# Performance work log

Measured on AMD Instinct MI355X. Metric: run time of the kernel, lower is better.

Reference implementation:

```python
import jax, jax.numpy as jnp
import numpy as np

B, C, KC, H, W, M = 8, 512, 256, 128, 128, 19


def _cbr(x, Wt, s, b):
    # 1x1 conv (no bias) + folded BatchNorm affine + ReLU.  x: [B,Cin,H,W], Wt: [Cout,Cin]
    y = jnp.einsum('oc,bchw->bohw', Wt, x)
    return jax.nn.relu(y * s[None, :, None, None] + b[None, :, None, None])


def setup_inputs() -> dict:
    key = jax.random.key(0)
    ks = jax.random.split(key, 10)
    inp = {
        'x': jax.random.normal(ks[0], (B, C, H, W), jnp.float32),
        'proxy': jax.random.normal(ks[1], (B, C, M, 1), jnp.float32),
    }
    # fan-in scaled weights so activations stay O(1)
    inp['W_p1'] = jax.random.normal(ks[2], (KC, C), jnp.float32) * (C ** -0.5)
    inp['W_p2'] = jax.random.normal(ks[3], (KC, KC), jnp.float32) * (KC ** -0.5)
    inp['W_o1'] = jax.random.normal(ks[4], (KC, C), jnp.float32) * (C ** -0.5)
    inp['W_o2'] = jax.random.normal(ks[5], (KC, KC), jnp.float32) * (KC ** -0.5)
    inp['W_d1'] = jax.random.normal(ks[6], (KC, C), jnp.float32) * (C ** -0.5)
    inp['W_d2'] = jax.random.normal(ks[7], (KC, KC), jnp.float32) * (KC ** -0.5)
    inp['W_u'] = jax.random.normal(ks[8], (C, KC), jnp.float32) * (KC ** -0.5)
    for name, dim in [('p1', KC), ('p2', KC), ('o1', KC), ('o2', KC), ('d1', KC), ('d2', KC), ('u', C)]:
        inp['s_' + name] = jnp.ones((dim,), jnp.float32)
        inp['b_' + name] = jnp.zeros((dim,), jnp.float32)
    return inp


def reference(x, proxy, W_p1, s_p1, b_p1, W_p2, s_p2, b_p2,
              W_o1, s_o1, b_o1, W_o2, s_o2, b_o2,
              W_d1, s_d1, b_d1, W_d2, s_d2, b_d2,
              W_u, s_u, b_u):
    b, _, h, w = x.shape
    kc = W_p1.shape[0]
    # pixel query / object key / object value projections (two ConvBnRelu each)
    q = _cbr(_cbr(x, W_p1, s_p1, b_p1), W_p2, s_p2, b_p2)          # [B,KC,H,W]
    k = _cbr(_cbr(proxy, W_o1, s_o1, b_o1), W_o2, s_o2, b_o2)      # [B,KC,M,1]
    v = _cbr(_cbr(proxy, W_d1, s_d1, b_d1), W_d2, s_d2, b_d2)      # [B,KC,M,1]
    q = q.reshape(b, kc, h * w)                                    # [B,KC,P]
    k = k.reshape(b, kc, -1)                                       # [B,KC,M]
    v = v.reshape(b, kc, -1)                                       # [B,KC,M]
    sim = jnp.einsum('bkp,bkm->bpm', q, k) * (kc ** -0.5)          # [B,P,M]
    sim = jax.nn.softmax(sim, axis=-1)
    ctx = jnp.einsum('bpm,bkm->bkp', sim, v).reshape(b, kc, h, w)  # [B,KC,H,W]
    return _cbr(ctx, W_u, s_u, b_u)                                # [B,C,H,W]
```

## Files before the change

### kernel.cpp

```cpp
#include <hip/hip_runtime.h>
#include <hip/hip_bf16.h>
#include <cstddef>
#include <cstdint>

constexpr int B_  = 8;
constexpr int C_  = 512;
constexpr int KC_ = 256;
constexpr int M_  = 19;
constexpr int P_  = 128 * 128;

typedef short frag8 __attribute__((ext_vector_type(8)));
typedef float f32x4 __attribute__((ext_vector_type(4)));
typedef unsigned short u16x8 __attribute__((ext_vector_type(8)));

__device__ __forceinline__ unsigned pk_bf16(float a, float b) {
    union { __hip_bfloat162 h; unsigned u; } cv;
    cv.h = __float22bfloat162_rn(make_float2(a, b));
    return cv.u;
}
__device__ __forceinline__ ushort bf16_1(float a) {
    union { __hip_bfloat16 h; ushort u; } cv;
    cv.h = __float2bfloat16(a);
    return cv.u;
}
__device__ __forceinline__ float bf16_f(ushort u) {
    return __uint_as_float(((unsigned)u) << 16);
}

__device__ __forceinline__ void gll16(const ushort* g, ushort* l) {
    __builtin_amdgcn_global_load_lds(
        (__attribute__((address_space(1))) void*)(ushort*)g,
        (__attribute__((address_space(3))) void*)l, 16, 0, 0);
}

__device__ __forceinline__ void two_stage_proj(
    const float* __restrict__ pS, float* __restrict__ t1,
    const float* __restrict__ W1, const float* __restrict__ s1, const float* __restrict__ b1,
    const float* __restrict__ W2, const float* __restrict__ s2, const float* __restrict__ b2,
    float* __restrict__ outg, int b, int tid)
{
    float acc[M_];
#pragma unroll
    for (int m = 0; m < M_; ++m) acc[m] = 0.f;
    const float4* wrow = reinterpret_cast<const float4*>(W1 + (size_t)tid * C_);
    for (int c4 = 0; c4 < C_ / 4; ++c4) {
        float4 w = wrow[c4];
        const float* pr = pS + c4 * 4 * M_;
#pragma unroll
        for (int m = 0; m < M_; ++m) acc[m] = fmaf(w.x, pr[m], acc[m]);
#pragma unroll
        for (int m = 0; m < M_; ++m) acc[m] = fmaf(w.y, pr[M_ + m], acc[m]);
#pragma unroll
        for (int m = 0; m < M_; ++m) acc[m] = fmaf(w.z, pr[2 * M_ + m], acc[m]);
#pragma unroll
        for (int m = 0; m < M_; ++m) acc[m] = fmaf(w.w, pr[3 * M_ + m], acc[m]);
    }
    float s = s1[tid], bb = b1[tid];
    __syncthreads();
#pragma unroll
    for (int m = 0; m < M_; ++m) t1[tid * M_ + m] = fmaxf(fmaf(acc[m], s, bb), 0.f);
    __syncthreads();
#pragma unroll
    for (int m = 0; m < M_; ++m) acc[m] = 0.f;
    const float4* wrow2 = reinterpret_cast<const float4*>(W2 + (size_t)tid * KC_);
    for (int c4 = 0; c4 < KC_ / 4; ++c4) {
        float4 w = wrow2[c4];
        const float* tr = t1 + c4 * 4 * M_;
#pragma unroll
        for (int m = 0; m < M_; ++m) acc[m] = fmaf(w.x, tr[m], acc[m]);
#pragma unroll
        for (int m = 0; m < M_; ++m) acc[m] = fmaf(w.y, tr[M_ + m], acc[m]);
#pragma unroll
        for (int m = 0; m < M_; ++m) acc[m] = fmaf(w.z, tr[2 * M_ + m], acc[m]);
#pragma unroll
        for (int m = 0; m < M_; ++m) acc[m] = fmaf(w.w, tr[3 * M_ + m], acc[m]);
    }
    s = s2[tid]; bb = b2[tid];
#pragma unroll
    for (int m = 0; m < M_; ++m)
        outg[((size_t)b * KC_ + tid) * M_ + m] = fmaxf(fmaf(acc[m], s, bb), 0.f);
}

__device__ __forceinline__ void cvt_w(const float* __restrict__ s, ushort* __restrict__ d,
                                      int n4, int cid, int nb) {
    for (int i = cid * 256 + (int)threadIdx.x; i < n4; i += nb * 256) {
        float4 f = ((const float4*)s)[i];
        ushort4 h;
        h.x = bf16_1(f.x); h.y = bf16_1(f.y); h.z = bf16_1(f.z); h.w = bf16_1(f.w);
        ((ushort4*)d)[i] = h;
    }
}

__global__ __launch_bounds__(256) void front_kernel(
    const float* __restrict__ proxy,
    const float* __restrict__ Wo1, const float* __restrict__ so1, const float* __restrict__ bo1,
    const float* __restrict__ Wo2, const float* __restrict__ so2, const float* __restrict__ bo2,
    const float* __restrict__ Wd1, const float* __restrict__ sd1, const float* __restrict__ bd1,
    const float* __restrict__ Wd2, const float* __restrict__ sd2, const float* __restrict__ bd2,
    float* __restrict__ Kg, float* __restrict__ Vg,
    const float* __restrict__ Wp1f, const float* __restrict__ Wp2f, const float* __restrict__ Wuf,
    ushort* __restrict__ Wp1b, ushort* __restrict__ Wp2b, ushort* __restrict__ Wub)
{
    __shared__ float pS[C_ * M_];
    __shared__ float t1[KC_ * M_];
    const int bx = blockIdx.x, tid = threadIdx.x;
    if (bx < 16) {
        const int b = bx >> 1;
        for (int i = tid; i < C_ * M_; i += 256) pS[i] = proxy[(size_t)b * C_ * M_ + i];
        __syncthreads();
        if (bx & 1)
            two_stage_proj(pS, t1, Wd1, sd1, bd1, Wd2, sd2, bd2, Vg, b, tid);
        else
            two_stage_proj(pS, t1, Wo1, so1, bo1, Wo2, so2, bo2, Kg, b, tid);
    } else {
        const int cid = bx - 16, nb = (int)gridDim.x - 16;
        cvt_w(Wp1f, Wp1b, KC_ * C_ / 4, cid, nb);
        cvt_w(Wp2f, Wp2b, KC_ * KC_ / 4, cid, nb);
        cvt_w(Wuf,  Wub,  C_ * KC_ / 4, cid, nb);
    }
}

__global__ __launch_bounds__(256) void cbr_f32in(
    const ushort* __restrict__ Wb, const float* __restrict__ X,
    const float* __restrict__ sc, const float* __restrict__ bi,
    ushort* __restrict__ Y)
{
    constexpr int K = C_;
    constexpr int O = KC_;
    __shared__ __align__(16) ushort As[128][40];
    __shared__ __align__(16) ushort Bs[128][40];

    const int tid = threadIdx.x;
    const unsigned bid = blockIdx.x;
    const unsigned swz = (bid & 7) * (gridDim.x >> 3) + (bid >> 3);
    const int m0 = (int)(swz & 1) * 128;
    const int n0 = (int)((swz >> 1) & 127) * 128;
    const int b  = (int)(swz >> 8);

    const int wave = tid >> 6, lane = tid & 63;
    const int quad = lane >> 4, l15 = lane & 15;
    const int mq = (wave & 1) * 64, nq = (wave >> 1) * 64;

    const int am  = tid >> 1;
    const int akh = (tid & 1) * 16;
    const int pp  = (tid & 63) * 2;
    const int bkg = (tid >> 6) * 8;

    const ushort* Wp = Wb + (size_t)(m0 + am) * K + akh;
    const float*  Xf = X + (size_t)b * K * P_ + n0 + pp;

    f32x4 acc[4][4];
#pragma unroll
    for (int i = 0; i < 4; ++i)
#pragma unroll
        for (int j = 0; j < 4; ++j) acc[i][j] = {0.f, 0.f, 0.f, 0.f};

    for (int k0 = 0; k0 < K; k0 += 32) {
        u16x8 wa0 = *(const u16x8*)(Wp + k0);
        u16x8 wa1 = *(const u16x8*)(Wp + k0 + 8);
        float2 xr[8];
#pragma unroll
        for (int j = 0; j < 8; ++j)
            xr[j] = *(const float2*)(Xf + (size_t)(k0 + bkg + j) * P_);
        unsigned bd0[4], bd1[4];
#pragma unroll
        for (int i = 0; i < 4; ++i) {
            bd0[i] = pk_bf16(xr[2 * i].x, xr[2 * i + 1].x);
            bd1[i] = pk_bf16(xr[2 * i].y, xr[2 * i + 1].y);
        }

        __syncthreads();
        *(u16x8*)(&As[am][akh])     = wa0;
        *(u16x8*)(&As[am][akh + 8]) = wa1;
        *(int4*)(&Bs[pp][bkg])      = *(int4*)bd0;
        *(int4*)(&Bs[pp + 1][bkg])  = *(int4*)bd1;
        __syncthreads();

        frag8 af[4], bfv[4];
#pragma unroll
        for (int f = 0; f < 4; ++f) {
            af[f]  = *(const frag8*)(&As[mq + f * 16 + l15][quad * 8]);
            bfv[f] = *(const frag8*)(&Bs[nq + f * 16 + l15][quad * 8]);
        }
#pragma unroll
        for (int i = 0; i < 4; ++i)
#pragma unroll
            for (int j = 0; j < 4; ++j)
                acc[i][j] = __builtin_amdgcn_mfma_f32_16x16x32_bf16(
                    af[i], bfv[j], acc[i][j], 0, 0, 0);
    }

#pragma unroll
    for (int i = 0; i < 4; ++i) {
        const int o0 = m0 + mq + i * 16 + quad * 4;
        float s4[4], b4[4];
#pragma unroll
        for (int r = 0; r < 4; ++r) { s4[r] = sc[o0 + r]; b4[r] = bi[o0 + r]; }
#pragma unroll
        for (int j = 0; j < 4; ++j) {
            const int p = n0 + nq + j * 16 + l15;
            float v0 = fmaxf(fmaf(acc[i][j][0], s4[0], b4[0]), 0.f);
            float v1 = fmaxf(fmaf(acc[i][j][1], s4[1], b4[1]), 0.f);
            float v2 = fmaxf(fmaf(acc[i][j][2], s4[2], b4[2]), 0.f);
            float v3 = fmaxf(fmaf(acc[i][j][3], s4[3], b4[3]), 0.f);
            uint2 w; w.x = pk_bf16(v0, v1); w.y = pk_bf16(v2, v3);
            *(uint2*)(Y + ((size_t)b * P_ + p) * O + o0) = w;
        }
    }
}

template <int K, int MT, bool OUT_F32>
__global__ __launch_bounds__(256) void cbr_bf16in(
    const ushort* __restrict__ Wb, const ushort* __restrict__ X,
    const float* __restrict__ sc, const float* __restrict__ bi,
    void* __restrict__ Yv)
{
    constexpr int O = MT * 128;
    __shared__ __align__(16) ushort As[2][4096];
    __shared__ __align__(16) ushort Bs[2][4096];

    const int tid = threadIdx.x;
    const unsigned bid = blockIdx.x;
    const unsigned swz = (bid & 7) * (gridDim.x >> 3) + (bid >> 3);
    const int m0 = (int)(swz % MT) * 128;
    const int n0 = (int)((swz / MT) & 127) * 128;
    const int b  = (int)(swz / (MT * 128));

    const int wave = tid >> 6, lane = tid & 63;
    const int quad = lane >> 4, l15 = lane & 15;
    const int mq = (wave & 1) * 64, nq = (wave >> 1) * 64;

    const int row = tid >> 1;
    const int jx  = (tid & 1) ^ ((tid >> 3) & 1);
    const ushort* aW = Wb + (size_t)(m0 + row) * K + jx * 8;
    const ushort* aX = X + ((size_t)b * P_ + n0 + row) * K + jx * 8;

    f32x4 acc[4][4];
#pragma unroll
    for (int i = 0; i < 4; ++i)
#pragma unroll
        for (int j = 0; j < 4; ++j) acc[i][j] = {0.f, 0.f, 0.f, 0.f};

    auto stage = [&](int buf, int k0) {
        const ushort* ga = aW + k0;
        const ushort* gb = aX + k0;
        ushort* la = &As[buf][wave * 512];
        ushort* lb = &Bs[buf][wave * 512];
        gll16(ga,      la);
        gll16(ga + 16, la + 2048);
        gll16(gb,      lb);
        gll16(gb + 16, lb + 2048);
    };

    stage(0, 0);
    __syncthreads();

    const int xb = (quad >> 1) * 2048 + ((((quad & 1) ^ ((l15 >> 2) & 1))) << 3);

    constexpr int NSTEP = K / 32;
#pragma unroll
    for (int t = 0; t < NSTEP; ++t) {
        if (t + 1 < NSTEP) stage((t + 1) & 1, (t + 1) * 32);
        const ushort* as = &As[t & 1][0];
        const ushort* bs = &Bs[t & 1][0];
        frag8 af[4], bfv[4];
#pragma unroll
        for (int f = 0; f < 4; ++f) {
            af[f]  = *(const frag8*)(as + xb + (mq + f * 16 + l15) * 16);
            bfv[f] = *(const frag8*)(bs + xb + (nq + f * 16 + l15) * 16);
        }
#pragma unroll
        for (int i = 0; i < 4; ++i)
#pragma unroll
            for (int j = 0; j < 4; ++j)
                acc[i][j] = __builtin_amdgcn_mfma_f32_16x16x32_bf16(
                    af[i], bfv[j], acc[i][j], 0, 0, 0);
        __syncthreads();
    }

#pragma unroll
    for (int i = 0; i < 4; ++i) {
        const int o0 = m0 + mq + i * 16 + quad * 4;
        float s4[4], b4[4];
#pragma unroll
        for (int r = 0; r < 4; ++r) { s4[r] = sc[o0 + r]; b4[r] = bi[o0 + r]; }
#pragma unroll
        for (int j = 0; j < 4; ++j) {
            const int p = n0 + nq + j * 16 + l15;
            float v0 = fmaxf(fmaf(acc[i][j][0], s4[0], b4[0]), 0.f);
            float v1 = fmaxf(fmaf(acc[i][j][1], s4[1], b4[1]), 0.f);
            float v2 = fmaxf(fmaf(acc[i][j][2], s4[2], b4[2]), 0.f);
            float v3 = fmaxf(fmaf(acc[i][j][3], s4[3], b4[3]), 0.f);
            if constexpr (OUT_F32) {
                float* Yf = (float*)Yv;
                Yf[((size_t)b * O + o0 + 0) * P_ + p] = v0;
                Yf[((size_t)b * O + o0 + 1) * P_ + p] = v1;
                Yf[((size_t)b * O + o0 + 2) * P_ + p] = v2;
                Yf[((size_t)b * O + o0 + 3) * P_ + p] = v3;
            } else {
                uint2 w; w.x = pk_bf16(v0, v1); w.y = pk_bf16(v2, v3);
                *(uint2*)((ushort*)Yv + ((size_t)b * P_ + p) * O + o0) = w;
            }
        }
    }
}

__global__ __launch_bounds__(256) void attn_kernel(
    ushort* __restrict__ Q, const float* __restrict__ Kg, const float* __restrict__ Vg)
{
    __shared__ float kS[KC_ * M_];
    __shared__ float vS[KC_ * M_];
    const int b = blockIdx.y;
    const int p = blockIdx.x * 256 + threadIdx.x;
    for (int i = threadIdx.x; i < KC_ * M_; i += 256) {
        kS[i] = Kg[(size_t)b * KC_ * M_ + i];
        vS[i] = Vg[(size_t)b * KC_ * M_ + i];
    }
    __syncthreads();

    u16x8* Qr = reinterpret_cast<u16x8*>(Q + ((size_t)b * P_ + p) * KC_);

    float s[M_];
#pragma unroll
    for (int m = 0; m < M_; ++m) s[m] = 0.f;

    for (int g = 0; g < KC_ / 8; ++g) {
        u16x8 u = Qr[g];
#pragma unroll
        for (int e = 0; e < 8; ++e) {
            float q = bf16_f((ushort)u[e]);
            const float* kr = kS + (g * 8 + e) * M_;
#pragma unroll
            for (int m = 0; m < M_; ++m) s[m] = fmaf(q, kr[m], s[m]);
        }
    }

    float mx = -1e30f;
#pragma unroll
    for (int m = 0; m < M_; ++m) { s[m] *= 0.0625f; mx = fmaxf(mx, s[m]); }
    float sum = 0.f;
#pragma unroll
    for (int m = 0; m < M_; ++m) { s[m] = __expf(s[m] - mx); sum += s[m]; }
    const float inv = 1.f / sum;
#pragma unroll
    for (int m = 0; m < M_; ++m) s[m] *= inv;

    for (int g = 0; g < KC_ / 8; ++g) {
        u16x8 o;
#pragma unroll
        for (int e = 0; e < 8; ++e) {
            const float* vr = vS + (g * 8 + e) * M_;
            float a = 0.f;
#pragma unroll
            for (int m = 0; m < M_; ++m) a = fmaf(s[m], vr[m], a);
            o[e] = (short)bf16_1(a);
        }
        Qr[g] = o;
    }
}

extern "C" void kernel_launch(void* const* d_in, const int* in_sizes, int n_in,
                              void* d_out, int out_size, void* d_ws, size_t ws_size,
                              hipStream_t stream)
{
    const float* x     = (const float*)d_in[0];
    const float* proxy = (const float*)d_in[1];
    const float* W_p1  = (const float*)d_in[2];
    const float* W_p2  = (const float*)d_in[3];
    const float* W_o1  = (const float*)d_in[4];
    const float* W_o2  = (const float*)d_in[5];
    const float* W_d1  = (const float*)d_in[6];
    const float* W_d2  = (const float*)d_in[7];
    const float* W_u   = (const float*)d_in[8];
    const float* s_p1  = (const float*)d_in[9];  const float* b_p1 = (const float*)d_in[10];
    const float* s_p2  = (const float*)d_in[11]; const float* b_p2 = (const float*)d_in[12];
    const float* s_o1  = (const float*)d_in[13]; const float* b_o1 = (const float*)d_in[14];
    const float* s_o2  = (const float*)d_in[15]; const float* b_o2 = (const float*)d_in[16];
    const float* s_d1  = (const float*)d_in[17]; const float* b_d1 = (const float*)d_in[18];
    const float* s_d2  = (const float*)d_in[19]; const float* b_d2 = (const float*)d_in[20];
    const float* s_u   = (const float*)d_in[21]; const float* b_u  = (const float*)d_in[22];

    float* out = (float*)d_out;
    float* Kg  = out;
    float* Vg  = Kg + (size_t)B_ * KC_ * M_;
    ushort* q1   = (ushort*)d_ws;
    ushort* q2   = q1 + (size_t)B_ * KC_ * P_;
    ushort* Wp1b = q2 + (size_t)B_ * KC_ * P_;
    ushort* Wp2b = Wp1b + (size_t)KC_ * C_;
    ushort* Wub  = Wp2b + (size_t)KC_ * KC_;

    front_kernel<<<dim3(176), dim3(256), 0, stream>>>(
        proxy, W_o1, s_o1, b_o1, W_o2, s_o2, b_o2,
               W_d1, s_d1, b_d1, W_d2, s_d2, b_d2, Kg, Vg,
        W_p1, W_p2, W_u, Wp1b, Wp2b, Wub);

    cbr_f32in<<<dim3(2 * 128 * B_), dim3(256), 0, stream>>>(
        Wp1b, x, s_p1, b_p1, q1);

    cbr_bf16in<KC_, 2, false><<<dim3(2 * 128 * B_), dim3(256), 0, stream>>>(
        Wp2b, q1, s_p2, b_p2, q2);

    attn_kernel<<<dim3(P_ / 256, B_), dim3(256), 0, stream>>>(q2, Kg, Vg);

    cbr_bf16in<KC_, 4, true><<<dim3(4 * 128 * B_), dim3(256), 0, stream>>>(
        Wub, q2, s_u, b_u, out);
}
```

Baseline: 793.4 us.

## Widen first projection GEMM tile to full output channels with pipelined loads

The f32-input projection kernel now uses 512-thread blocks that each cover all 256 output channels for a 128-pixel tile, so the fp32 activations of x are read and converted to bf16 once instead of twice. Weights are staged through double-buffered async global-to-LDS loads, and the next step's activation loads are prefetched behind explicit vmcnt waits and raw barriers. The bf16-input GEMM also swaps __syncthreads for finer-grained waitcnt plus barrier. This adds register and LDS pressure per block and depends on the hand-written waitcnt counts being correct.

```diff
diff --git a/kernel.cpp b/kernel.cpp
--- a/kernel.cpp
+++ b/kernel.cpp
@@ -120,34 +120,31 @@
     }
 }
 
-__global__ __launch_bounds__(256) void cbr_f32in(
+__global__ __launch_bounds__(512, 4) void cbr_f32in(
     const ushort* __restrict__ Wb, const float* __restrict__ X,
     const float* __restrict__ sc, const float* __restrict__ bi,
     ushort* __restrict__ Y)
 {
     constexpr int K = C_;
     constexpr int O = KC_;
-    __shared__ __align__(16) ushort As[128][40];
+    __shared__ __align__(16) ushort As[2][8192];
     __shared__ __align__(16) ushort Bs[128][40];
 
     const int tid = threadIdx.x;
     const unsigned bid = blockIdx.x;
     const unsigned swz = (bid & 7) * (gridDim.x >> 3) + (bid >> 3);
-    const int m0 = (int)(swz & 1) * 128;
-    const int n0 = (int)((swz >> 1) & 127) * 128;
-    const int b  = (int)(swz >> 8);
+    const int n0 = (int)(swz & 127) * 128;
+    const int b  = (int)(swz >> 7);
 
     const int wave = tid >> 6, lane = tid & 63;
     const int quad = lane >> 4, l15 = lane & 15;
-    const int mq = (wave & 1) * 64, nq = (wave >> 1) * 64;
-
-    const int am  = tid >> 1;
-    const int akh = (tid & 1) * 16;
-    const int pp  = (tid & 63) * 2;
-    const int bkg = (tid >> 6) * 8;
-
-    const ushort* Wp = Wb + (size_t)(m0 + am) * K + akh;
-    const float*  Xf = X + (size_t)b * K * P_ + n0 + pp;
+    const int mq = (wave >> 1) * 64, nq = (wave & 1) * 64;
+
+    const int jx = (tid & 1) ^ ((tid >> 3) & 1);
+    const ushort* aW = Wb + (size_t)(tid >> 1) * K + jx * 8;
+    const int pp = (tid & 63) * 2;
+    const int kg = (tid >> 6) * 4;
+    const float* Xf = X + (size_t)b * K * P_ + n0 + pp;
 
     f32x4 acc[4][4];
 #pragma unroll
@@ -155,31 +152,46 @@
 #pragma unroll
         for (int j = 0; j < 4; ++j) acc[i][j] = {0.f, 0.f, 0.f, 0.f};
 
-    for (int k0 = 0; k0 < K; k0 += 32) {
-        u16x8 wa0 = *(const u16x8*)(Wp + k0);
-        u16x8 wa1 = *(const u16x8*)(Wp + k0 + 8);
-        float2 xr[8];
-#pragma unroll
-        for (int j = 0; j < 8; ++j)
-            xr[j] = *(const float2*)(Xf + (size_t)(k0 + bkg + j) * P_);
-        unsigned bd0[4], bd1[4];
-#pragma unroll
-        for (int i = 0; i < 4; ++i) {
-            bd0[i] = pk_bf16(xr[2 * i].x, xr[2 * i + 1].x);
-            bd1[i] = pk_bf16(xr[2 * i].y, xr[2 * i + 1].y);
-        }
-
-        __syncthreads();
-        *(u16x8*)(&As[am][akh])     = wa0;
-        *(u16x8*)(&As[am][akh + 8]) = wa1;
-        *(int4*)(&Bs[pp][bkg])      = *(int4*)bd0;
-        *(int4*)(&Bs[pp + 1][bkg])  = *(int4*)bd1;
-        __syncthreads();
-
+    float2 xr[4];
+    auto loadB = [&](int k0) {
+#pragma unroll
+        for (int j = 0; j < 4; ++j)
+            xr[j] = *(const float2*)(Xf + (size_t)(k0 + kg + j) * P_);
+    };
+    auto stageA = [&](int buf, int k0) {
+        const ushort* g = aW + k0;
+        ushort* l = &As[buf][wave * 512];
+        gll16(g,      l);
+        gll16(g + 16, l + 4096);
+    };
+
+    loadB(0);
+    stageA(0, 0);
+    const int axb = (quad >> 1) * 4096 + ((((quad & 1) ^ ((l15 >> 2) & 1))) << 3);
+
+    auto body = [&](int t, bool pf) {
+        unsigned bd0[2], bd1[2];
+        bd0[0] = pk_bf16(xr[0].x, xr[1].x); bd0[1] = pk_bf16(xr[2].x, xr[3].x);
+        bd1[0] = pk_bf16(xr[0].y, xr[1].y); bd1[1] = pk_bf16(xr[2].y, xr[3].y);
+        asm volatile("s_waitcnt lgkmcnt(0)" ::: "memory");
+        __builtin_amdgcn_s_barrier();
+        *(uint2*)(&Bs[pp][kg])     = *(uint2*)bd0;
+        *(uint2*)(&Bs[pp + 1][kg]) = *(uint2*)bd1;
+        if (pf) {
+            loadB((t + 1) * 32);
+            stageA((t + 1) & 1, (t + 1) * 32);
+            asm volatile("s_waitcnt vmcnt(6)" ::: "memory");
+        } else {
+            asm volatile("s_waitcnt vmcnt(0)" ::: "memory");
+        }
+        asm volatile("s_waitcnt lgkmcnt(0)" ::: "memory");
+        __builtin_amdgcn_s_barrier();
+
+        const ushort* as = &As[t & 1][0];
         frag8 af[4], bfv[4];
 #pragma unroll
         for (int f = 0; f < 4; ++f) {
-            af[f]  = *(const frag8*)(&As[mq + f * 16 + l15][quad * 8]);
+            af[f]  = *(const frag8*)(as + axb + (mq + f * 16 + l15) * 16);
             bfv[f] = *(const frag8*)(&Bs[nq + f * 16 + l15][quad * 8]);
         }
 #pragma unroll
@@ -188,11 +200,14 @@
             for (int j = 0; j < 4; ++j)
                 acc[i][j] = __builtin_amdgcn_mfma_f32_16x16x32_bf16(
                     af[i], bfv[j], acc[i][j], 0, 0, 0);
-    }
+    };
+
+    for (int t = 0; t < K / 32 - 1; ++t) body(t, true);
+    body(K / 32 - 1, false);
 
 #pragma unroll
     for (int i = 0; i < 4; ++i) {
-        const int o0 = m0 + mq + i * 16 + quad * 4;
+        const int o0 = mq + i * 16 + quad * 4;
         float s4[4], b4[4];
 #pragma unroll
         for (int r = 0; r < 4; ++r) { s4[r] = sc[o0 + r]; b4[r] = bi[o0 + r]; }
@@ -253,14 +268,20 @@
     };
 
     stage(0, 0);
-    __syncthreads();
 
     const int xb = (quad >> 1) * 2048 + ((((quad & 1) ^ ((l15 >> 2) & 1))) << 3);
 
     constexpr int NSTEP = K / 32;
 #pragma unroll
     for (int t = 0; t < NSTEP; ++t) {
-        if (t + 1 < NSTEP) stage((t + 1) & 1, (t + 1) * 32);
+        if (t + 1 < NSTEP) {
+            stage((t + 1) & 1, (t + 1) * 32);
+            asm volatile("s_waitcnt vmcnt(4)" ::: "memory");
+        } else {
+            asm volatile("s_waitcnt vmcnt(0)" ::: "memory");
+        }
+        __builtin_amdgcn_s_barrier();
+
         const ushort* as = &As[t & 1][0];
         const ushort* bs = &Bs[t & 1][0];
         frag8 af[4], bfv[4];
@@ -275,7 +296,9 @@
             for (int j = 0; j < 4; ++j)
                 acc[i][j] = __builtin_amdgcn_mfma_f32_16x16x32_bf16(
                     af[i], bfv[j], acc[i][j], 0, 0, 0);
-        __syncthreads();
+
+        asm volatile("s_waitcnt lgkmcnt(0)" ::: "memory");
+        __builtin_amdgcn_s_barrier();
     }
 
 #pragma unroll
@@ -394,7 +417,7 @@
                W_d1, s_d1, b_d1, W_d2, s_d2, b_d2, Kg, Vg,
         W_p1, W_p2, W_u, Wp1b, Wp2b, Wub);
 
-    cbr_f32in<<<dim3(2 * 128 * B_), dim3(256), 0, stream>>>(
+    cbr_f32in<<<dim3(128 * B_), dim3(512), 0, stream>>>(
         Wp1b, x, s_p1, b_p1, q1);
 
     cbr_bf16in<KC_, 2, false><<<dim3(2 * 128 * B_), dim3(256), 0, stream>>>(
```

New measurement: 778.4 us. About the same (-1.9%).
